# Performance work log

Hardware: AMD Instinct MI355X
Metric: run time of the kernel (lower is better)

## Reference

```python
import jax, jax.numpy as jnp
import numpy as np

B, T, C, H = 2, 2048, 384, 6
HD = C // H
SINK_ITERS = 6  # MAX_ITER_SINK
EPS_LN = 1e-5


def layer_norm(x, w, b):
    mu = jnp.mean(x, axis=-1, keepdims=True)
    var = jnp.var(x, axis=-1, keepdims=True)
    return (x - mu) * jax.lax.rsqrt(var + EPS_LN) * w + b


def sinkhorn(c):
    # Log-domain Sinkhorn (sinkformers SinkhornDistance, eps=1, uniform 1/T marginals).
    # c: (B,H,T,T) row-softmaxed attention. C_cost=-c so M(C,u,v)= c + u_i + v_j.
    logT = jnp.log(jnp.asarray(T, c.dtype))
    u = jnp.zeros(c.shape[:-1], c.dtype)  # (B,H,T)
    v = jnp.zeros(c.shape[:-1], c.dtype)
    for i in range(SINK_ITERS):
        if i % 2 == 0:
            u = u - logT - jax.nn.logsumexp(c + u[..., :, None] + v[..., None, :], axis=-1)
        else:
            v = v - logT - jax.nn.logsumexp(c + u[..., :, None] + v[..., None, :], axis=-2)
            v = jax.lax.stop_gradient(v)  # torch code detaches v each odd iter
    return jnp.exp(c + u[..., :, None] + v[..., None, :])


def setup_inputs() -> dict:
    key = jax.random.key(0)
    ks = jax.random.split(key, 8)
    s = 0.02
    return {
        "x": jax.random.normal(ks[0], (B, T, C), jnp.float32),
        "t": jax.random.uniform(ks[1], (1,), jnp.float32),
        "ln1_w": jnp.ones((C + 1,), jnp.float32),
        "ln1_b": jnp.zeros((C + 1,), jnp.float32),
        "attn_w": (jax.random.normal(ks[2], (C + 1, 3 * C), jnp.float32) * s),  # torch W.T
        "attn_b": jnp.zeros((3 * C,), jnp.float32),
        "proj_w": (jax.random.normal(ks[3], (C, C), jnp.float32) * s),
        "proj_b": jnp.zeros((C,), jnp.float32),
        "ln2_w": jnp.ones((C + 1,), jnp.float32),
        "ln2_b": jnp.zeros((C + 1,), jnp.float32),
        "fc_w": (jax.random.normal(ks[4], (C + 1, 4 * C), jnp.float32) * s),
        "fc_b": jnp.zeros((4 * C,), jnp.float32),
        "fc2_w": (jax.random.normal(ks[5], (4 * C, C), jnp.float32) * s),
        "fc2_b": jnp.zeros((C,), jnp.float32),
    }


def add_time(h, t):
    b, tt, _ = h.shape
    tcol = jnp.broadcast_to(t.reshape(1, 1, 1).astype(h.dtype), (b, tt, 1))
    return jnp.concatenate([h, tcol], axis=-1)


def reference(x, t, ln1_w, ln1_b, attn_w, attn_b, proj_w, proj_b,
              ln2_w, ln2_b, fc_w, fc_b, fc2_w, fc2_b):
    # ---- attention sub-block ----
    xt = add_time(x, t)                       # (B,T,C+1)
    xn = layer_norm(xt, ln1_w, ln1_b)
    qkv = xn @ attn_w + attn_b                # (B,T,3C)
    q, k, vv = jnp.split(qkv, 3, axis=-1)
    q = q.reshape(B, T, H, HD).transpose(0, 2, 1, 3)   # (B,H,T,HD)
    k = k.reshape(B, T, H, HD).transpose(0, 2, 1, 3)
    vv = vv.reshape(B, T, H, HD).transpose(0, 2, 1, 3)
    att = jnp.einsum('bhqd,bhkd->bhqk', q, k) * (1.0 / np.sqrt(HD))
    causal = jnp.tril(jnp.ones((T, T), bool))
    att = jnp.where(causal, att, -jnp.inf)
    att = jax.nn.softmax(att, axis=-1)
    pi = sinkhorn(att) * T                    # sinked_att * last-dim size
    y = jnp.einsum('bhqk,bhkd->bhqd', pi, vv)
    y = y.transpose(0, 2, 1, 3).reshape(B, T, C)
    h = y @ proj_w + proj_b                   # (B,T,C)
    # ---- MLP sub-block ----
    ht = add_time(h, t)
    hn = layer_norm(ht, ln2_w, ln2_b)
    m = jax.nn.gelu(hn @ fc_w + fc_b, approximate=False)
    o = m @ fc2_w + fc2_b
    return o
```

## Files before the change

### kernel.cpp

```cpp
#include <hip/hip_runtime.h>
#include <hip/hip_fp16.h>
#include <math.h>

#define B 2
#define T 2048
#define C 384
#define H 6
#define HD 64
#define BHT (B*H*T)
#define LOGT 7.6246189861593985f

typedef __half half_t;
typedef _Float16 f16x8 __attribute__((ext_vector_type(8)));
typedef float f32x4 __attribute__((ext_vector_type(4)));

__device__ __forceinline__ float block_reduce_sum(float v) {
    __shared__ float sm[4];
    int lane = threadIdx.x & 63, wid = threadIdx.x >> 6;
#pragma unroll
    for (int o = 32; o > 0; o >>= 1) v += __shfl_down(v, o, 64);
    __syncthreads();
    if (lane == 0) sm[wid] = v;
    __syncthreads();
    return sm[0] + sm[1] + sm[2] + sm[3];
}

__device__ __forceinline__ float wave_allreduce_sum(float v) {
#pragma unroll
    for (int o = 1; o < 64; o <<= 1) v += __shfl_xor(v, o, 64);
    return v;
}

__global__ __launch_bounds__(256) void zerof_kernel(float* __restrict__ p) {
    p[(size_t)blockIdx.x * 256 + threadIdx.x] = 0.f;
}

__global__ __launch_bounds__(256) void addtime_ln_f16(
        const float* __restrict__ src, const float* __restrict__ tptr,
        const float* __restrict__ w, const float* __restrict__ bb,
        _Float16* __restrict__ dst, int KP) {
    const int n = C + 1;
    int row = blockIdx.x;
    const float* srow = src + (size_t)row * C;
    float tval = tptr[0];
    int i0 = threadIdx.x;
    int i1 = threadIdx.x + 256;
    float v0 = srow[i0];
    bool has1 = (i1 < n);
    float v1 = 0.f;
    if (has1) v1 = (i1 < C) ? srow[i1] : tval;
    float s  = block_reduce_sum(v0 + v1);
    float sq = block_reduce_sum(v0*v0 + v1*v1);
    float mean = s / n;
    float var  = sq / n - mean * mean;
    float rstd = rsqrtf(var + 1e-5f);
    _Float16* drow = dst + (size_t)row * KP;
    drow[i0] = (_Float16)((v0 - mean) * rstd * w[i0] + bb[i0]);
    if (has1) drow[i1] = (_Float16)((v1 - mean) * rstd * w[i1] + bb[i1]);
    else if (i1 < KP) drow[i1] = (_Float16)0.f;
}

__global__ __launch_bounds__(256) void convtrans_kernel(const float* __restrict__ W,
        _Float16* __restrict__ Wt, int K, int N, int KP) {
    __shared__ float tile[32][33];
    int k0 = blockIdx.x * 32, n0 = blockIdx.y * 32;
    int tx = threadIdx.x & 31, ty = threadIdx.x >> 5;
#pragma unroll
    for (int i = 0; i < 4; ++i) {
        int k = k0 + ty + i * 8, n = n0 + tx;
        tile[ty + i * 8][tx] = (k < K && n < N) ? W[(size_t)k * N + n] : 0.f;
    }
    __syncthreads();
#pragma unroll
    for (int i = 0; i < 4; ++i) {
        int n = n0 + ty + i * 8, k = k0 + tx;
        if (n < N && k < KP) Wt[(size_t)n * KP + k] = (_Float16)tile[tx][ty + i * 8];
    }
}

__device__ __forceinline__ f16x8 load8(const _Float16* p) { return *(const f16x8*)p; }
__device__ __forceinline__ f16x8 load8(const float* p) {
    float4 a = *(const float4*)p, b2 = *(const float4*)(p + 4);
    f16x8 r;
    r[0]=(_Float16)a.x; r[1]=(_Float16)a.y; r[2]=(_Float16)a.z; r[3]=(_Float16)a.w;
    r[4]=(_Float16)b2.x; r[5]=(_Float16)b2.y; r[6]=(_Float16)b2.z; r[7]=(_Float16)b2.w;
    return r;
}

template<int ACT, int QKV, typename AT, typename OUT_T>
__global__ __launch_bounds__(256) void mfma_gemm(
        const AT* __restrict__ A, const _Float16* __restrict__ Wt,
        const float* __restrict__ bias, OUT_T* __restrict__ out,
        int M, int N, int KP) {
    __shared__ __align__(16) _Float16 As[64][40];
    __shared__ __align__(16) _Float16 Bs[64][40];
    int tid = threadIdx.x;
    int lane = tid & 63, wave = tid >> 6;
    int wr = wave >> 1, wc = wave & 1;
    int m0 = blockIdx.y * 64, n0 = blockIdx.x * 64;
    int arow = tid >> 2, seg = tid & 3;
    int lrow = lane & 15, lseg = lane >> 4;
    f32x4 acc[2][2] = {};
    for (int k0 = 0; k0 < KP; k0 += 32) {
        __syncthreads();
        *(f16x8*)&As[arow][seg * 8] = load8(&A[(size_t)(m0 + arow) * KP + k0 + seg * 8]);
        *(f16x8*)&Bs[arow][seg * 8] = *(const f16x8*)&Wt[(size_t)(n0 + arow) * KP + k0 + seg * 8];
        __syncthreads();
        f16x8 af[2], bf[2];
#pragma unroll
        for (int i = 0; i < 2; ++i) af[i] = *(const f16x8*)&As[wr*32 + i*16 + lrow][lseg*8];
#pragma unroll
        for (int j = 0; j < 2; ++j) bf[j] = *(const f16x8*)&Bs[wc*32 + j*16 + lrow][lseg*8];
#pragma unroll
        for (int i = 0; i < 2; ++i)
#pragma unroll
            for (int j = 0; j < 2; ++j)
                acc[i][j] = __builtin_amdgcn_mfma_f32_16x16x32_f16(af[i], bf[j], acc[i][j], 0, 0, 0);
    }
    int lcol = lane & 15, lr4 = (lane >> 4) * 4;
#pragma unroll
    for (int i = 0; i < 2; ++i)
#pragma unroll
        for (int j = 0; j < 2; ++j) {
            int col = n0 + wc * 32 + j * 16 + lcol;
            float bv = bias[col];
#pragma unroll
            for (int r = 0; r < 4; ++r) {
                int row = m0 + wr * 32 + i * 16 + lr4 + r;
                float v = acc[i][j][r] + bv;
                if (ACT == 1) v = 0.5f * v * (1.f + erff(v * 0.70710678118654752f));
                if (QKV) {
                    int wq = col / C;
                    int rem = col - wq * C;
                    int hh = rem >> 6, dd = rem & 63;
                    int bb2 = row >> 11, tt = row & 2047;
                    out[(((size_t)wq * (B*H) + bb2 * H + hh) * T + tt) * 64 + dd] = (OUT_T)v;
                } else {
                    out[(size_t)row * N + col] = (OUT_T)v;
                }
            }
        }
}

template<int ACT, int QKV, typename AT, typename OUT_T>
__global__ __launch_bounds__(256) void mfma_gemm128(
        const AT* __restrict__ A, const _Float16* __restrict__ Wt,
        const float* __restrict__ bias, OUT_T* __restrict__ out,
        int M, int N, int KP) {
    __shared__ __align__(16) _Float16 As[128][40];
    __shared__ __align__(16) _Float16 Bs[128][40];
    int tid = threadIdx.x;
    int lane = tid & 63, wave = tid >> 6;
    int wr = wave >> 1, wc = wave & 1;
    int m0 = blockIdx.y * 128, n0 = blockIdx.x * 128;
    int lrow = lane & 15, lseg = lane >> 4;
    f32x4 acc[4][4] = {};
    for (int k0 = 0; k0 < KP; k0 += 32) {
        __syncthreads();
#pragma unroll
        for (int it = 0; it < 2; ++it) {
            int r = (tid >> 2) + it * 64, sg = tid & 3;
            *(f16x8*)&As[r][sg * 8] = load8(&A[(size_t)(m0 + r) * KP + k0 + sg * 8]);
            *(f16x8*)&Bs[r][sg * 8] = *(const f16x8*)&Wt[(size_t)(n0 + r) * KP + k0 + sg * 8];
        }
        __syncthreads();
        f16x8 af[4], bf[4];
#pragma unroll
        for (int i = 0; i < 4; ++i) af[i] = *(const f16x8*)&As[wr*64 + i*16 + lrow][lseg*8];
#pragma unroll
        for (int j = 0; j < 4; ++j) bf[j] = *(const f16x8*)&Bs[wc*64 + j*16 + lrow][lseg*8];
#pragma unroll
        for (int i = 0; i < 4; ++i)
#pragma unroll
            for (int j = 0; j < 4; ++j)
                acc[i][j] = __builtin_amdgcn_mfma_f32_16x16x32_f16(af[i], bf[j], acc[i][j], 0, 0, 0);
    }
    int lcol = lane & 15, lr4 = (lane >> 4) * 4;
#pragma unroll
    for (int i = 0; i < 4; ++i)
#pragma unroll
        for (int j = 0; j < 4; ++j) {
            int col = n0 + wc * 64 + j * 16 + lcol;
            float bv = bias[col];
#pragma unroll
            for (int r = 0; r < 4; ++r) {
                int row = m0 + wr * 64 + i * 16 + lr4 + r;
                float v = acc[i][j][r] + bv;
                if (ACT == 1) v = 0.5f * v * (1.f + erff(v * 0.70710678118654752f));
                if (QKV) {
                    int wq = col / C;
                    int rem = col - wq * C;
                    int hh = rem >> 6, dd = rem & 63;
                    int bb2 = row >> 11, tt = row & 2047;
                    out[(((size_t)wq * (B*H) + bb2 * H + hh) * T + tt) * 64 + dd] = (OUT_T)v;
                } else {
                    out[(size_t)row * N + col] = (OUT_T)v;
                }
            }
        }
}

__global__ __launch_bounds__(256) void qk_tileA(const _Float16* __restrict__ qh,
        const _Float16* __restrict__ kh, half_t* __restrict__ c_h) {
    int p = blockIdx.x, bh = blockIdx.y;
    int qt = (int)((sqrtf(8.f * (float)p + 1.f) - 1.f) * 0.5f);
    while ((qt + 1) * (qt + 2) / 2 <= p) ++qt;
    while (qt * (qt + 1) / 2 > p) --qt;
    int jt = p - qt * (qt + 1) / 2;
    int tid = threadIdx.x, lane = tid & 63, wave = tid >> 6;
    int wr = wave >> 1, wc = wave & 1;
    int lrow = lane & 15, lseg = lane >> 4;
    int orow = (lane >> 4) * 4, ocol = lane & 15;
    __shared__ __align__(16) _Float16 Qs[64][72];
    __shared__ __align__(16) _Float16 Ks[64][72];
    const _Float16* qb = qh + ((size_t)bh * T + qt * 64) * 64;
    const _Float16* kb = kh + ((size_t)bh * T + jt * 64) * 64;
#pragma unroll
    for (int k = 0; k < 2; ++k) {
        int cc = k * 256 + tid;
        int r = cc >> 3, sg = cc & 7;
        *(f16x8*)&Qs[r][sg*8] = *(const f16x8*)&qb[r*64 + sg*8];
        *(f16x8*)&Ks[r][sg*8] = *(const f16x8*)&kb[r*64 + sg*8];
    }
    __syncthreads();
    f32x4 acc[2][2] = {};
    f16x8 af[2], bf[2];
#pragma unroll
    for (int i = 0; i < 2; ++i) af[i] = *(const f16x8*)&Qs[wr*32+i*16+lrow][lseg*8];
#pragma unroll
    for (int j = 0; j < 2; ++j) bf[j] = *(const f16x8*)&Ks[wc*32+j*16+lrow][lseg*8];
#pragma unroll
    for (int i = 0; i < 2; ++i)
#pragma unroll
        for (int j = 0; j < 2; ++j)
            acc[i][j] = __builtin_amdgcn_mfma_f32_16x16x32_f16(af[i], bf[j], acc[i][j], 0,0,0);
#pragma unroll
    for (int i = 0; i < 2; ++i) af[i] = *(const f16x8*)&Qs[wr*32+i*16+lrow][32+lseg*8];
#pragma unroll
    for (int j = 0; j < 2; ++j) bf[j] = *(const f16x8*)&Ks[wc*32+j*16+lrow][32+lseg*8];
#pragma unroll
    for (int i = 0; i < 2; ++i)
#pragma unroll
        for (int j = 0; j < 2; ++j)
            acc[i][j] = __builtin_amdgcn_mfma_f32_16x16x32_f16(af[i], bf[j], acc[i][j], 0,0,0);
    __syncthreads();
    bool diag = (qt == jt);
#pragma unroll
    for (int i = 0; i < 2; ++i)
#pragma unroll
        for (int r = 0; r < 4; ++r) {
            int rl = wr*32 + i*16 + orow + r;
#pragma unroll
            for (int j = 0; j < 2; ++j) {
                int cl = wc*32 + j*16 + ocol;
                float s = acc[i][j][r] * 0.125f;
                float e = (diag && cl > rl) ? 0.f : __expf(s);
                Ks[rl][cl] = (_Float16)e;
            }
        }
    __syncthreads();
    half_t* cb = c_h + ((size_t)bh * T + qt * 64) * T + jt * 64;
#pragma unroll
    for (int k = 0; k < 2; ++k) {
        int cc = k * 256 + tid;
        int r = cc >> 3, sg = cc & 7;
        *(uint4*)&cb[(size_t)r * T + sg*8] = *(const uint4*)&Ks[r][sg*8];
    }
}

__global__ __launch_bounds__(256) void norm_q_col(half_t* __restrict__ c_h,
        float* __restrict__ eu, float* __restrict__ cacc) {
    int qt = 31 - (blockIdx.x >> 1), half = blockIdx.x & 1, bh = blockIdx.y;
    int tid = threadIdx.x, lane = tid & 63, w = tid >> 6;
    int span = (qt + 1) * 64, nch = span >> 3;
    __shared__ float colacc[4][2048];
    float acc32[32];
#pragma unroll
    for (int k = 0; k < 32; ++k) acc32[k] = 0.f;
    half_t* cb = c_h + ((size_t)bh * T + qt * 64 + half * 32) * T;
    for (int rr = 0; rr < 8; ++rr) {
        int i = w * 8 + rr;
        half_t* crow = cb + (size_t)i * T;
        uint4 raw[4];
        float z = 0.f;
#pragma unroll
        for (int k = 0; k < 4; ++k) {
            int ch = lane + (k << 6);
            if (ch < nch) {
                uint4 rw = *(const uint4*)(crow + ch * 8);
                raw[k] = rw;
                const __half2* h2 = (const __half2*)&rw;
#pragma unroll
                for (int pp = 0; pp < 4; ++pp) {
                    float2 cf = __half22float2(h2[pp]);
                    z += cf.x + cf.y;
                }
            }
        }
        z = wave_allreduce_sum(z);
        float inv = 1.f / z;
        float qv[32];
        float S = 0.f;
#pragma unroll
        for (int k = 0; k < 4; ++k) {
            int ch = lane + (k << 6);
            if (ch < nch) {
                const __half2* h2 = (const __half2*)&raw[k];
                union { __half2 h[4]; uint4 u; } ou;
#pragma unroll
                for (int pp = 0; pp < 4; ++pp) {
                    float2 cf = __half22float2(h2[pp]);
                    float q0 = __expf(cf.x * inv), q1 = __expf(cf.y * inv);
                    S += q0 + q1;
                    qv[k*8+pp*2] = q0; qv[k*8+pp*2+1] = q1;
                    ou.h[pp] = __floats2half2_rn(q0, q1);
                }
                *(uint4*)(crow + ch * 8) = ou.u;
            }
        }
        S = wave_allreduce_sum(S);
        float eui = 1.f / (2048.f * (S + (float)(T - span)));
        if (lane == 0) eu[(size_t)bh * T + qt * 64 + half * 32 + i] = eui;
#pragma unroll
        for (int k = 0; k < 4; ++k) {
            int ch = lane + (k << 6);
            if (ch < nch)
#pragma unroll
                for (int e = 0; e < 8; ++e)
                    acc32[k*8+e] = fmaf(qv[k*8+e], eui, acc32[k*8+e]);
        }
    }
#pragma unroll
    for (int k = 0; k < 4; ++k) {
        int ch = lane + (k << 6);
        if (ch < nch)
#pragma unroll
            for (int e = 0; e < 8; ++e)
                colacc[w][ch*8+e] = acc32[k*8+e];
    }
    __syncthreads();
    for (int j = tid; j < span; j += 256)
        atomicAdd(&cacc[(size_t)bh*T + j],
                  colacc[0][j]+colacc[1][j]+colacc[2][j]+colacc[3][j]);
}

__global__ __launch_bounds__(256) void row_col(const half_t* __restrict__ c_h,
        const float* __restrict__ ev, const float* __restrict__ sev,
        float* __restrict__ eu, float* __restrict__ cacc) {
    int qt = 31 - (blockIdx.x >> 1), half = blockIdx.x & 1, bh = blockIdx.y;
    int tid = threadIdx.x, lane = tid & 63, w = tid >> 6;
    int span = (qt + 1) * 64, nch = span >> 3;
    __shared__ float colacc[4][2048];
    float evreg[32], acc32[32];
#pragma unroll
    for (int k = 0; k < 32; ++k) acc32[k] = 0.f;
    const float* evb = ev + (size_t)bh * T;
#pragma unroll
    for (int k = 0; k < 4; ++k) {
        int ch = lane + (k << 6);
        if (ch < nch) {
            float4 e0 = *(const float4*)(evb + ch*8);
            float4 e1 = *(const float4*)(evb + ch*8 + 4);
            evreg[k*8+0]=e0.x; evreg[k*8+1]=e0.y; evreg[k*8+2]=e0.z; evreg[k*8+3]=e0.w;
            evreg[k*8+4]=e1.x; evreg[k*8+5]=e1.y; evreg[k*8+6]=e1.z; evreg[k*8+7]=e1.w;
        }
    }
    float tail = sev[bh*33 + qt + 1];
    const half_t* cb = c_h + ((size_t)bh * T + qt * 64 + half * 32) * T;
    for (int rr = 0; rr < 8; ++rr) {
        int i = w * 8 + rr;
        const half_t* crow = cb + (size_t)i * T;
        uint4 raw[4];
        float s = 0.f;
#pragma unroll
        for (int k = 0; k < 4; ++k) {
            int ch = lane + (k << 6);
            if (ch < nch) {
                uint4 rw = *(const uint4*)(crow + ch * 8);
                raw[k] = rw;
                const __half2* h2 = (const __half2*)&rw;
#pragma unroll
                for (int pp = 0; pp < 4; ++pp) {
                    float2 cf = __half22float2(h2[pp]);
                    s = fmaf(cf.x, evreg[k*8+pp*2],   s);
                    s = fmaf(cf.y, evreg[k*8+pp*2+1], s);
                }
            }
        }
        s = wave_allreduce_sum(s);
        float eui = 1.f / (2048.f * (s + tail));
        if (lane == 0) eu[(size_t)bh * T + qt * 64 + half * 32 + i] = eui;
#pragma unroll
        for (int k = 0; k < 4; ++k) {
            int ch = lane + (k << 6);
            if (ch < nch) {
                const __half2* h2 = (const __half2*)&raw[k];
#pragma unroll
                for (int pp = 0; pp < 4; ++pp) {
                    float2 cf = __half22float2(h2[pp]);
                    acc32[k*8+pp*2]   = fmaf(cf.x, eui, acc32[k*8+pp*2]);
                    acc32[k*8+pp*2+1] = fmaf(cf.y, eui, acc32[k*8+pp*2+1]);
                }
            }
        }
    }
#pragma unroll
    for (int k = 0; k < 4; ++k) {
        int ch = lane + (k << 6);
        if (ch < nch)
#pragma unroll
            for (int e = 0; e < 8; ++e)
                colacc[w][ch*8+e] = acc32[k*8+e];
    }
    __syncthreads();
    for (int j = tid; j < span; j += 256)
        atomicAdd(&cacc[(size_t)bh*T + j],
                  colacc[0][j]+colacc[1][j]+colacc[2][j]+colacc[3][j]);
}

__global__ __launch_bounds__(256) void v_fin_full(float* __restrict__ cacc,
        const float* __restrict__ eu, float* __restrict__ ev,
        float* __restrict__ sev) {
    int bh = blockIdx.x;
    int tid = threadIdx.x;
    __shared__ float part[256];
    __shared__ float pre[33];
    __shared__ float ts2[32];
    const float* eub = eu + (size_t)bh * T;
    float* caccb = cacc + (size_t)bh * T;
    float* evb = ev + (size_t)bh * T;
    float a = 0.f;
#pragma unroll
    for (int e = 0; e < 8; ++e) a += eub[tid*8 + e];
    part[tid] = a;
    __syncthreads();
    if (tid == 0) {
        float run = 0.f;
        for (int kt = 0; kt < 32; ++kt) {
            pre[kt] = run;
            float t0 = 0.f;
            for (int k = 0; k < 8; ++k) t0 += part[kt*8 + k];
            run += t0;
        }
        pre[32] = run;
    }
    __syncthreads();
    float p = pre[tid >> 3];
    float b2 = 0.f;
#pragma unroll
    for (int e = 0; e < 8; ++e) {
        int j = tid*8 + e;
        float vj = 1.f / (2048.f * (caccb[j] + p));
        evb[j] = vj;
        caccb[j] = 0.f;
        b2 += vj;
    }
    part[tid] = b2;
    __syncthreads();
    if (tid < 32) {
        float t0 = 0.f;
#pragma unroll
        for (int k = 0; k < 8; ++k) t0 += part[tid*8 + k];
        ts2[tid] = t0;
    }
    __syncthreads();
    if (tid == 0) {
        float run = 0.f;
        sev[bh*33 + 32] = 0.f;
        for (int kt = 31; kt >= 0; --kt) { run += ts2[kt]; sev[bh*33 + kt] = run; }
    }
}

__global__ __launch_bounds__(256) void wv_suffix_kernel(const _Float16* __restrict__ vh,
        const float* __restrict__ ev, float* __restrict__ wsuf) {
    int bh = blockIdx.x;
    int tid = threadIdx.x;
    int d = tid & 63, g = tid >> 6;
    __shared__ float evs[2048];
    __shared__ float W[32][64];
    __shared__ float red[4][64];
    const float* vb = ev + (size_t)bh * T;
#pragma unroll
    for (int k = 0; k < 8; ++k) evs[tid + k*256] = vb[tid + k*256];
    __syncthreads();
    const _Float16* vbase = vh + (size_t)bh * T * 64;
    for (int jt = 0; jt < 32; ++jt) {
        float a = 0.f;
#pragma unroll
        for (int jj = 0; jj < 16; ++jj) {
            int j = jt*64 + g*16 + jj;
            a += evs[j] * (float)vbase[(size_t)j * 64 + d];
        }
        red[g][d] = a;
        __syncthreads();
        if (g == 0) W[jt][d] = red[0][d] + red[1][d] + red[2][d] + red[3][d];
        __syncthreads();
    }
    if (tid < 64) {
        float run = 0.f;
        wsuf[((size_t)bh*33 + 32)*64 + tid] = 0.f;
        for (int kt = 31; kt >= 0; --kt) {
            run += W[kt][tid];
            wsuf[((size_t)bh*33 + kt)*64 + tid] = run;
        }
    }
}

__global__ __launch_bounds__(256) void pv_split(const half_t* __restrict__ c_h,
        const float* __restrict__ eu, const float* __restrict__ ev,
        const _Float16* __restrict__ vh, const float* __restrict__ wsuf,
        float* __restrict__ y32) {
    int qt = (T/64 - 1) - blockIdx.x, kc = blockIdx.y, bh = blockIdx.z;
    int j0 = kc * 8;
    if (j0 > qt) return;
    int jend = min(qt + 1, j0 + 8);
    int b = bh / H, h = bh - b * H;
    int tid = threadIdx.x, lane = tid & 63, wave = tid >> 6;
    int wr = wave >> 1, wc = wave & 1;
    int lrow = lane & 15, lseg = lane >> 4;
    int orow = (lane >> 4) * 4, ocol = lane & 15;
    __shared__ __align__(16) _Float16 Ps[64][72];
    __shared__ __align__(16) _Float16 Vt[64][72];
    __shared__ float facs[64], vs[64], wsf[64];
    if (tid < 64) {
        facs[tid] = eu[(size_t)bh*T + qt*64 + tid] * 2048.f;
        if (kc == 0) wsf[tid] = wsuf[((size_t)bh*33 + qt + 1)*64 + tid];
    }
    f32x4 acc[2][2] = {};
    const half_t* cb0 = c_h + ((size_t)bh*T + qt*64)*T;
    for (int jt = j0; jt < jend; ++jt) {
        __syncthreads();
        if (tid < 64) vs[tid] = ev[(size_t)bh*T + jt*64 + tid];
        __syncthreads();
#pragma unroll
        for (int k = 0; k < 2; ++k) {
            int cc = k*256 + tid;
            int r = cc >> 3, sg = cc & 7;
            uint4 rw = *(const uint4*)&cb0[(size_t)r*T + jt*64 + sg*8];
            const __half2* h2 = (const __half2*)&rw;
            float fr = facs[r];
            f16x8 p8;
#pragma unroll
            for (int pp = 0; pp < 4; ++pp) {
                float2 cf = __half22float2(h2[pp]);
                p8[pp*2]   = (_Float16)(cf.x * fr * vs[sg*8 + pp*2]);
                p8[pp*2+1] = (_Float16)(cf.y * fr * vs[sg*8 + pp*2 + 1]);
            }
            *(f16x8*)&Ps[r][sg*8] = p8;
        }
        {
            const _Float16* vb = vh + ((size_t)bh*T + jt*64)*64;
#pragma unroll
            for (int k = 0; k < 2; ++k) {
                int d8 = (wave*2 + k) * 8;
                f16x8 v8 = *(const f16x8*)&vb[(size_t)lane*64 + d8];
#pragma unroll
                for (int e = 0; e < 8; ++e) Vt[d8 + e][lane] = v8[e];
            }
        }
        __syncthreads();
        f16x8 af[2], bf[2];
#pragma unroll
        for (int i = 0; i < 2; ++i) af[i] = *(const f16x8*)&Ps[wr*32+i*16+lrow][lseg*8];
#pragma unroll
        for (int j = 0; j < 2; ++j) bf[j] = *(const f16x8*)&Vt[wc*32+j*16+lrow][lseg*8];
#pragma unroll
        for (int i = 0; i < 2; ++i)
#pragma unroll
            for (int j = 0; j < 2; ++j)
                acc[i][j] = __builtin_amdgcn_mfma_f32_16x16x32_f16(af[i], bf[j], acc[i][j], 0,0,0);
#pragma unroll
        for (int i = 0; i < 2; ++i) af[i] = *(const f16x8*)&Ps[wr*32+i*16+lrow][32+lseg*8];
#pragma unroll
        for (int j = 0; j < 2; ++j) bf[j] = *(const f16x8*)&Vt[wc*32+j*16+lrow][32+lseg*8];
#pragma unroll
        for (int i = 0; i < 2; ++i)
#pragma unroll
            for (int j = 0; j < 2; ++j)
                acc[i][j] = __builtin_amdgcn_mfma_f32_16x16x32_f16(af[i], bf[j], acc[i][j], 0,0,0);
    }
#pragma unroll
    for (int i = 0; i < 2; ++i)
#pragma unroll
        for (int j = 0; j < 2; ++j)
#pragma unroll
            for (int r = 0; r < 4; ++r) {
                int rl = wr*32 + i*16 + orow + r;
                int cl = wc*32 + j*16 + ocol;
                float val = acc[i][j][r];
                if (kc == 0) val += facs[rl] * wsf[cl];
                atomicAdd(&y32[((size_t)b*T + qt*64 + rl)*C + h*HD + cl], val);
            }
}

extern "C" void kernel_launch(void* const* d_in, const int* in_sizes, int n_in,
                              void* d_out, int out_size, void* d_ws, size_t ws_size,
                              hipStream_t stream) {
    (void)in_sizes; (void)n_in; (void)out_size;
    const float* x      = (const float*)d_in[0];
    const float* t      = (const float*)d_in[1];
    const float* ln1_w  = (const float*)d_in[2];
    const float* ln1_b  = (const float*)d_in[3];
    const float* attn_w = (const float*)d_in[4];
    const float* attn_b = (const float*)d_in[5];
    const float* proj_w = (const float*)d_in[6];
    const float* proj_b = (const float*)d_in[7];
    const float* ln2_w  = (const float*)d_in[8];
    const float* ln2_b  = (const float*)d_in[9];
    const float* fc_w   = (const float*)d_in[10];
    const float* fc_b   = (const float*)d_in[11];
    const float* fc2_w  = (const float*)d_in[12];
    const float* fc2_b  = (const float*)d_in[13];
    float* out = (float*)d_out;

    if (ws_size < 121482240ull) return;
    char* wsb = (char*)d_ws;
    half_t*    c_h  = (half_t*)wsb;
    _Float16*  qkvh = (_Float16*)(wsb + 100663296ull);
    float*     y32  = (float*)(wsb + 110100480ull);
    _Float16*  xh   = (_Float16*)(wsb + 116391936ull);
    _Float16*  wbuf = (_Float16*)(wsb + 119799808ull);
    float*     eu   = (float*)(wsb + 121077760ull);
    float*     ev   = eu   + BHT;
    float*     cacc = ev   + BHT;
    float*     sev  = cacc + BHT;
    float*     wsuf = sev  + 1024;
    const _Float16* qh = qkvh;
    const _Float16* kh = qkvh + (size_t)(B*H) * T * 64;
    const _Float16* vh = qkvh + (size_t)2 * (B*H) * T * 64;
    _Float16* xn_h = xh;
    _Float16* hn_h = xh;
    float*    hb   = (float*)qkvh;
    _Float16* mb_h = (_Float16*)wsb;

    const int M = B * T;
    const int KP1 = 416;

    addtime_ln_f16<<<M, 256, 0, stream>>>(x, t, ln1_w, ln1_b, xn_h, KP1);
    convtrans_kernel<<<dim3(KP1/32, (3*C)/32), 256, 0, stream>>>(attn_w, wbuf, C+1, 3*C, KP1);
    mfma_gemm128<0, 1, _Float16, _Float16><<<dim3(3*C/128, M/128), 256, 0, stream>>>(
        xn_h, wbuf, attn_b, qkvh, M, 3*C, KP1);
    qk_tileA<<<dim3(528, B*H), 256, 0, stream>>>(qh, kh, c_h);

    zerof_kernel<<<BHT/256, 256, 0, stream>>>(cacc);
    norm_q_col<<<dim3(64, B*H), 256, 0, stream>>>(c_h, eu, cacc);
    v_fin_full<<<B*H, 256, 0, stream>>>(cacc, eu, ev, sev);
    row_col<<<dim3(64, B*H), 256, 0, stream>>>(c_h, ev, sev, eu, cacc);
    v_fin_full<<<B*H, 256, 0, stream>>>(cacc, eu, ev, sev);
    row_col<<<dim3(64, B*H), 256, 0, stream>>>(c_h, ev, sev, eu, cacc);
    v_fin_full<<<B*H, 256, 0, stream>>>(cacc, eu, ev, sev);

    wv_suffix_kernel<<<B*H, 256, 0, stream>>>(vh, ev, wsuf);
    zerof_kernel<<<(M*C)/256, 256, 0, stream>>>(y32);
    pv_split<<<dim3(T/64, 4, B*H), 256, 0, stream>>>(c_h, eu, ev, vh, wsuf, y32);

    convtrans_kernel<<<dim3(C/32, C/32), 256, 0, stream>>>(proj_w, wbuf, C, C, C);
    mfma_gemm<0, 0, float, float><<<dim3(C/64, M/64), 256, 0, stream>>>(
        y32, wbuf, proj_b, hb, M, C, C);

    addtime_ln_f16<<<M, 256, 0, stream>>>(hb, t, ln2_w, ln2_b, hn_h, KP1);
    convtrans_kernel<<<dim3(KP1/32, (4*C)/32), 256, 0, stream>>>(fc_w, wbuf, C+1, 4*C, KP1);
    mfma_gemm128<1, 0, _Float16, _Float16><<<dim3(4*C/128, M/128), 256, 0, stream>>>(
        hn_h, wbuf, fc_b, mb_h, M, 4*C, KP1);
    convtrans_kernel<<<dim3((4*C)/32, C/32), 256, 0, stream>>>(fc2_w, wbuf, 4*C, C, 4*C);
    mfma_gemm<0, 0, _Float16, float><<<dim3(C/64, M/64), 256, 0, stream>>>(
        mb_h, wbuf, fc2_b, out, M, C, 4*C);
}
```

Baseline: 323.3 us.

## Fuse final Sinkhorn v-update with wv suffix, drop split-K atomics in PV

Zeroing of the column accumulator moves into qk_tileA, and the final v_fin_full is fused with the V-weighted suffix kernel, which removes several small launches. The PV kernel no longer splits over key chunks with atomicAdd into an fp32 buffer. Each block now loops over all key tiles for its query tile and writes fp16 output directly, which also removes the y32 zero-fill. The projection GEMM then reads fp16 input. The trade-off is fewer, longer-running blocks with an imbalanced causal workload, and fp16 rounding of the attention output.

```diff
diff --git a/kernel.cpp b/kernel.cpp
--- a/kernel.cpp
+++ b/kernel.cpp
@@ -29,10 +29,6 @@
 #pragma unroll
     for (int o = 1; o < 64; o <<= 1) v += __shfl_xor(v, o, 64);
     return v;
-}
-
-__global__ __launch_bounds__(256) void zerof_kernel(float* __restrict__ p) {
-    p[(size_t)blockIdx.x * 256 + threadIdx.x] = 0.f;
 }
 
 __global__ __launch_bounds__(256) void addtime_ln_f16(
@@ -201,8 +197,10 @@
 }
 
 __global__ __launch_bounds__(256) void qk_tileA(const _Float16* __restrict__ qh,
-        const _Float16* __restrict__ kh, half_t* __restrict__ c_h) {
+        const _Float16* __restrict__ kh, half_t* __restrict__ c_h,
+        float* __restrict__ cacc) {
     int p = blockIdx.x, bh = blockIdx.y;
+    if (p < 8) cacc[(size_t)bh * 2048 + p * 256 + threadIdx.x] = 0.f;
     int qt = (int)((sqrtf(8.f * (float)p + 1.f) - 1.f) * 0.5f);
     while ((qt + 1) * (qt + 2) / 2 <= p) ++qt;
     while (qt * (qt + 1) / 2 > p) --qt;
@@ -471,27 +469,54 @@
     }
 }
 
-__global__ __launch_bounds__(256) void wv_suffix_kernel(const _Float16* __restrict__ vh,
-        const float* __restrict__ ev, float* __restrict__ wsuf) {
+__global__ __launch_bounds__(256) void v_fin_wv(const float* __restrict__ cacc,
+        const float* __restrict__ eu, float* __restrict__ ev,
+        const _Float16* __restrict__ vh, float* __restrict__ wsuf) {
     int bh = blockIdx.x;
     int tid = threadIdx.x;
-    int d = tid & 63, g = tid >> 6;
+    __shared__ float part[256];
+    __shared__ float pre[33];
     __shared__ float evs[2048];
     __shared__ float W[32][64];
     __shared__ float red[4][64];
-    const float* vb = ev + (size_t)bh * T;
-#pragma unroll
-    for (int k = 0; k < 8; ++k) evs[tid + k*256] = vb[tid + k*256];
-    __syncthreads();
+    const float* eub = eu + (size_t)bh * T;
+    const float* caccb = cacc + (size_t)bh * T;
+    float* evb = ev + (size_t)bh * T;
+    float a = 0.f;
+#pragma unroll
+    for (int e = 0; e < 8; ++e) a += eub[tid*8 + e];
+    part[tid] = a;
+    __syncthreads();
+    if (tid == 0) {
+        float run = 0.f;
+        for (int kt = 0; kt < 32; ++kt) {
+            pre[kt] = run;
+            float t0 = 0.f;
+            for (int k = 0; k < 8; ++k) t0 += part[kt*8 + k];
+            run += t0;
+        }
+        pre[32] = run;
+    }
+    __syncthreads();
+    float p = pre[tid >> 3];
+#pragma unroll
+    for (int e = 0; e < 8; ++e) {
+        int j = tid*8 + e;
+        float vj = 1.f / (2048.f * (caccb[j] + p));
+        evb[j] = vj;
+        evs[j] = vj;
+    }
+    __syncthreads();
+    int d = tid & 63, g = tid >> 6;
     const _Float16* vbase = vh + (size_t)bh * T * 64;
     for (int jt = 0; jt < 32; ++jt) {
-        float a = 0.f;
+        float acc2 = 0.f;
 #pragma unroll
         for (int jj = 0; jj < 16; ++jj) {
             int j = jt*64 + g*16 + jj;
-            a += evs[j] * (float)vbase[(size_t)j * 64 + d];
-        }
-        red[g][d] = a;
+            acc2 += evs[j] * (float)vbase[(size_t)j * 64 + d];
+        }
+        red[g][d] = acc2;
         __syncthreads();
         if (g == 0) W[jt][d] = red[0][d] + red[1][d] + red[2][d] + red[3][d];
         __syncthreads();
@@ -506,14 +531,12 @@
     }
 }
 
-__global__ __launch_bounds__(256) void pv_split(const half_t* __restrict__ c_h,
+__global__ __launch_bounds__(256) void pv_full(const half_t* __restrict__ c_h,
         const float* __restrict__ eu, const float* __restrict__ ev,
         const _Float16* __restrict__ vh, const float* __restrict__ wsuf,
-        float* __restrict__ y32) {
-    int qt = (T/64 - 1) - blockIdx.x, kc = blockIdx.y, bh = blockIdx.z;
-    int j0 = kc * 8;
-    if (j0 > qt) return;
-    int jend = min(qt + 1, j0 + 8);
+        _Float16* __restrict__ y) {
+    int qt = 31 - blockIdx.x;
+    int bh = blockIdx.y;
     int b = bh / H, h = bh - b * H;
     int tid = threadIdx.x, lane = tid & 63, wave = tid >> 6;
     int wr = wave >> 1, wc = wave & 1;
@@ -521,21 +544,23 @@
     int orow = (lane >> 4) * 4, ocol = lane & 15;
     __shared__ __align__(16) _Float16 Ps[64][72];
     __shared__ __align__(16) _Float16 Vt[64][72];
-    __shared__ float facs[64], vs[64], wsf[64];
+    __shared__ float facs[64], wsf[64];
     if (tid < 64) {
         facs[tid] = eu[(size_t)bh*T + qt*64 + tid] * 2048.f;
-        if (kc == 0) wsf[tid] = wsuf[((size_t)bh*33 + qt + 1)*64 + tid];
-    }
+        wsf[tid]  = wsuf[((size_t)bh*33 + qt + 1)*64 + tid];
+    }
+    __syncthreads();
     f32x4 acc[2][2] = {};
     const half_t* cb0 = c_h + ((size_t)bh*T + qt*64)*T;
-    for (int jt = j0; jt < jend; ++jt) {
-        __syncthreads();
-        if (tid < 64) vs[tid] = ev[(size_t)bh*T + jt*64 + tid];
-        __syncthreads();
+    const float* evb = ev + (size_t)bh * T;
+    int sg = tid & 7;
+    for (int jt = 0; jt <= qt; ++jt) {
+        float4 e0 = *(const float4*)(evb + jt*64 + sg*8);
+        float4 e1 = *(const float4*)(evb + jt*64 + sg*8 + 4);
+        float er[8] = {e0.x,e0.y,e0.z,e0.w,e1.x,e1.y,e1.z,e1.w};
 #pragma unroll
         for (int k = 0; k < 2; ++k) {
-            int cc = k*256 + tid;
-            int r = cc >> 3, sg = cc & 7;
+            int r = ((k*256 + tid) >> 3);
             uint4 rw = *(const uint4*)&cb0[(size_t)r*T + jt*64 + sg*8];
             const __half2* h2 = (const __half2*)&rw;
             float fr = facs[r];
@@ -543,8 +568,8 @@
 #pragma unroll
             for (int pp = 0; pp < 4; ++pp) {
                 float2 cf = __half22float2(h2[pp]);
-                p8[pp*2]   = (_Float16)(cf.x * fr * vs[sg*8 + pp*2]);
-                p8[pp*2+1] = (_Float16)(cf.y * fr * vs[sg*8 + pp*2 + 1]);
+                p8[pp*2]   = (_Float16)(cf.x * fr * er[pp*2]);
+                p8[pp*2+1] = (_Float16)(cf.y * fr * er[pp*2+1]);
             }
             *(f16x8*)&Ps[r][sg*8] = p8;
         }
@@ -578,6 +603,7 @@
 #pragma unroll
             for (int j = 0; j < 2; ++j)
                 acc[i][j] = __builtin_amdgcn_mfma_f32_16x16x32_f16(af[i], bf[j], acc[i][j], 0,0,0);
+        __syncthreads();
     }
 #pragma unroll
     for (int i = 0; i < 2; ++i)
@@ -587,9 +613,8 @@
             for (int r = 0; r < 4; ++r) {
                 int rl = wr*32 + i*16 + orow + r;
                 int cl = wc*32 + j*16 + ocol;
-                float val = acc[i][j][r];
-                if (kc == 0) val += facs[rl] * wsf[cl];
-                atomicAdd(&y32[((size_t)b*T + qt*64 + rl)*C + h*HD + cl], val);
+                float val = acc[i][j][r] + facs[rl] * wsf[cl];
+                y[((size_t)b*T + qt*64 + rl)*C + h*HD + cl] = (_Float16)val;
             }
 }
 
@@ -625,10 +650,12 @@
     float*     cacc = ev   + BHT;
     float*     sev  = cacc + BHT;
     float*     wsuf = sev  + 1024;
+    (void)y32;
     const _Float16* qh = qkvh;
     const _Float16* kh = qkvh + (size_t)(B*H) * T * 64;
     const _Float16* vh = qkvh + (size_t)2 * (B*H) * T * 64;
     _Float16* xn_h = xh;
+    _Float16* yb_h = xh;
     _Float16* hn_h = xh;
     float*    hb   = (float*)qkvh;
     _Float16* mb_h = (_Float16*)wsb;
@@ -640,23 +667,20 @@
     convtrans_kernel<<<dim3(KP1/32, (3*C)/32), 256, 0, stream>>>(attn_w, wbuf, C+1, 3*C, KP1);
     mfma_gemm128<0, 1, _Float16, _Float16><<<dim3(3*C/128, M/128), 256, 0, stream>>>(
         xn_h, wbuf, attn_b, qkvh, M, 3*C, KP1);
-    qk_tileA<<<dim3(528, B*H), 256, 0, stream>>>(qh, kh, c_h);
-
-    zerof_kernel<<<BHT/256, 256, 0, stream>>>(cacc);
+    qk_tileA<<<dim3(528, B*H), 256, 0, stream>>>(qh, kh, c_h, cacc);
+
     norm_q_col<<<dim3(64, B*H), 256, 0, stream>>>(c_h, eu, cacc);
     v_fin_full<<<B*H, 256, 0, stream>>>(cacc, eu, ev, sev);
     row_col<<<dim3(64, B*H), 256, 0, stream>>>(c_h, ev, sev, eu, cacc);
     v_fin_full<<<B*H, 256, 0, stream>>>(cacc, eu, ev, sev);
     row_col<<<dim3(64, B*H), 256, 0, stream>>>(c_h, ev, sev, eu, cacc);
-    v_fin_full<<<B*H, 256, 0, stream>>>(cacc, eu, ev, sev);
-
-    wv_suffix_kernel<<<B*H, 256, 0, stream>>>(vh, ev, wsuf);
-    zerof_kernel<<<(M*C)/256, 256, 0, stream>>>(y32);
-    pv_split<<<dim3(T/64, 4, B*H), 256, 0, stream>>>(c_h, eu, ev, vh, wsuf, y32);
+    v_fin_wv<<<B*H, 256, 0, stream>>>(cacc, eu, ev, vh, wsuf);
+
+    pv_full<<<dim3(T/64, B*H), 256, 0, stream>>>(c_h, eu, ev, vh, wsuf, yb_h);
 
     convtrans_kernel<<<dim3(C/32, C/32), 256, 0, stream>>>(proj_w, wbuf, C, C, C);
-    mfma_gemm<0, 0, float, float><<<dim3(C/64, M/64), 256, 0, stream>>>(
-        y32, wbuf, proj_b, hb, M, C, C);
+    mfma_gemm<0, 0, _Float16, float><<<dim3(C/64, M/64), 256, 0, stream>>>(
+        yb_h, wbuf, proj_b, hb, M, C, C);
 
     addtime_ln_f16<<<M, 256, 0, stream>>>(hb, t, ln2_w, ln2_b, hn_h, KP1);
     convtrans_kernel<<<dim3(KP1/32, (4*C)/32), 256, 0, stream>>>(fc_w, wbuf, C+1, 4*C, KP1);
```

Result: slower. 342.4 us (+5.9%).
